# Performance work log

Hardware: AMD Instinct MI355X
Metric: run time of the kernel (lower is better)

The kernel has to match this reference:

```python
import jax, jax.numpy as jnp
import numpy as np

HIDDEN = 1024
HEADS = 16
DEPTH = HIDDEN // HEADS  # 64
B, F, T = 2, 2048, 2048


def setup_inputs() -> dict:
    key = jax.random.key(0)
    ks = jax.random.split(key, 7)
    return {
        "query_input": jax.random.normal(ks[0], (B, F, HIDDEN), dtype=jnp.float32),
        "source_input": jax.random.normal(ks[1], (B, T, HIDDEN), dtype=jnp.float32),
        "bias": jax.random.normal(ks[2], (1, 1, F, T), dtype=jnp.float32),
        "wq": jax.random.normal(ks[3], (HIDDEN, HEADS, DEPTH), dtype=jnp.float32) * 0.02,
        "wk": jax.random.normal(ks[4], (HIDDEN, HEADS, DEPTH), dtype=jnp.float32) * 0.02,
        "wv": jax.random.normal(ks[5], (HIDDEN, HEADS, DEPTH), dtype=jnp.float32) * 0.02,
        "wo": jax.random.normal(ks[6], (HEADS, DEPTH, HIDDEN), dtype=jnp.float32) * 0.02,
    }


def reference(query_input, source_input, bias, wq, wk, wv, wo):
    # projections: [B,S,C] x [C,N,H] -> [B,S,N,H]
    q = jnp.einsum("bfc,cnh->bfnh", query_input, wq)
    k = jnp.einsum("btc,cnh->btnh", source_input, wk)
    v = jnp.einsum("btc,cnh->btnh", source_input, wv)
    q = q * (DEPTH ** -0.5)
    # logits: [B,N,F,T], softmax over T (last dim)
    logits = jnp.einsum("btnh,bfnh->bnft", k, q)
    logits = logits + bias
    weights = jax.nn.softmax(logits, axis=3)
    attn = jnp.einsum("bnft,btnh->bfnh", weights, v)
    out = jnp.einsum("bfnh,nhe->bfe", attn, wo)
    return out
```

## Files before the change

kernel.cpp:

```cpp
#include <hip/hip_runtime.h>

#define LOG2E 1.44269504f

typedef __attribute__((ext_vector_type(8))) short short8v;
typedef __attribute__((ext_vector_type(4))) float f32x4;
typedef unsigned int u32;
typedef __attribute__((address_space(1))) const u32* gp_t;
typedef __attribute__((address_space(3))) u32* lp_t;

#define MFMA(a, b, c) __builtin_amdgcn_mfma_f32_16x16x32_bf16((a), (b), (c), 0, 0, 0)

__device__ __forceinline__ unsigned short f2bf(float f) {
  unsigned int u = __float_as_uint(f);
  u = (u + 0x7fffu + ((u >> 16) & 1u)) >> 16;
  return (unsigned short)u;
}
__device__ __forceinline__ u32 cvtpk(float lo, float hi) {
  u32 r;
  asm("v_cvt_pk_bf16_f32 %0, %1, %2" : "=v"(r) : "v"(lo), "v"(hi));
  return r;
}

__global__ void k_cvt2(const float* __restrict__ a, const float* __restrict__ bsrc,
                       unsigned short* __restrict__ oa, unsigned short* __restrict__ ob,
                       int n4each) {
  int stride = gridDim.x * blockDim.x;
  for (int i = blockIdx.x * blockDim.x + threadIdx.x; i < 2 * n4each; i += stride) {
    bool second = i >= n4each;
    int j = second ? i - n4each : i;
    float4 v = second ? reinterpret_cast<const float4*>(bsrc)[j]
                      : reinterpret_cast<const float4*>(a)[j];
    ushort4 o;
    o.x = f2bf(v.x); o.y = f2bf(v.y); o.z = f2bf(v.z); o.w = f2bf(v.w);
    (second ? reinterpret_cast<ushort4*>(ob) : reinterpret_cast<ushort4*>(oa))[j] = o;
  }
}

__global__ void k_cvt_t4(const float* __restrict__ w0, const float* __restrict__ w1,
                         const float* __restrict__ w2, const float* __restrict__ w3,
                         unsigned short* __restrict__ wqkvT, unsigned short* __restrict__ woT) {
  __shared__ float tile[32][33];
  int z = blockIdx.z;
  const float* in = (z == 0) ? w0 : (z == 1) ? w1 : (z == 2) ? w2 : w3;
  unsigned short* out = (z < 3) ? (wqkvT + (size_t)z * 1048576) : woT;
  float scale = (z == 0) ? 0.125f * LOG2E : 1.0f;
  int bx = blockIdx.x * 32, by = blockIdx.y * 32;
  int tx = threadIdx.x, ty = threadIdx.y;
  for (int r = ty; r < 32; r += 8)
    tile[r][tx] = in[(size_t)(by + r) * 1024 + bx + tx];
  __syncthreads();
  for (int r = ty; r < 32; r += 8)
    out[(size_t)(bx + r) * 1024 + by + tx] = f2bf(tile[tx][r] * scale);
}

__global__ void k_bias_perm(const float* __restrict__ in, float* __restrict__ out) {
  int bid = blockIdx.x;
  int fb = bid >> 5, ch = bid & 31;
  int tid = threadIdx.x;
  int tt = tid >> 6, rem = tid & 63;
  int g = rem >> 4, l15 = rem & 15;
  float4 v = *reinterpret_cast<const float4*>(
      &in[(size_t)(fb * 16 + l15) * 2048 + ch * 64 + tt * 16 + g * 4]);
  v.x *= LOG2E; v.y *= LOG2E; v.z *= LOG2E; v.w *= LOG2E;
  *reinterpret_cast<float4*>(&out[(size_t)bid * 1024 + tid * 4]) = v;
}

__global__ __launch_bounds__(256)
void k_gemmqkv(const unsigned short* __restrict__ Aq, const unsigned short* __restrict__ Asrc,
               const unsigned short* __restrict__ W,
               unsigned short* __restrict__ dq, unsigned short* __restrict__ dk,
               unsigned short* __restrict__ dv) {
  __shared__ __align__(16) unsigned short Al[2][8192];
  __shared__ __align__(16) unsigned short Bl[2][4096];
  const int tid = threadIdx.x;
  const int lane = tid & 63, wid = tid >> 6;
  const int g = lane >> 4, l15 = lane & 15, l7 = l15 & 7;
  const int wm = wid >> 1, wn = wid & 1;
  const int rowbase = blockIdx.y * 128;
  const int colbase = blockIdx.x * 64;
  const bool isV = colbase >= 2048;
  const unsigned short* A = (colbase < 1024) ? Aq : Asrc;
  const int xgl = (g ^ l7) << 4;

  const int jr = tid >> 3;
  const int sc = ((tid & 7) ^ (jr & 7)) << 3;
  const unsigned short* As0 = A + (size_t)(rowbase + jr) * 1024 + sc;
  const unsigned short* Ws0 = W + (size_t)(colbase + jr) * 1024 + sc;

  const f32x4 zf = {0.f, 0.f, 0.f, 0.f};
  f32x4 acc[4][2];
#pragma unroll
  for (int mf = 0; mf < 4; ++mf) { acc[mf][0] = zf; acc[mf][1] = zf; }

  auto stage = [&](int buf, int k0) {
    char* Ad = (char*)&Al[buf][0];
    char* Bd = (char*)&Bl[buf][0];
#pragma unroll
    for (int p = 0; p < 4; ++p)
      __builtin_amdgcn_global_load_lds((gp_t)(As0 + (size_t)p * 32 * 1024 + k0),
                                       (lp_t)(Ad + (p * 256 + tid) * 16), 16, 0, 0);
#pragma unroll
    for (int p = 0; p < 2; ++p)
      __builtin_amdgcn_global_load_lds((gp_t)(Ws0 + (size_t)p * 32 * 1024 + k0),
                                       (lp_t)(Bd + (p * 256 + tid) * 16), 16, 0, 0);
  };
  auto ldfrags = [&](int buf, int kk, short8v af[4], short8v bfr[2]) {
    const char* Ac = (const char*)&Al[buf][0];
    const char* Bc = (const char*)&Bl[buf][0];
#pragma unroll
    for (int mf = 0; mf < 4; ++mf)
      af[mf] = *reinterpret_cast<const short8v*>(
          Ac + ((wm * 64 + mf * 16 + l15) << 7) + (xgl ^ (kk << 6)));
#pragma unroll
    for (int nf = 0; nf < 2; ++nf)
      bfr[nf] = *reinterpret_cast<const short8v*>(
          Bc + ((wn * 32 + nf * 16 + l15) << 7) + (xgl ^ (kk << 6)));
  };

  stage(0, 0);
  __syncthreads();
#pragma unroll 1
  for (int s = 0; s < 16; ++s) {
    if (s < 15) stage((s + 1) & 1, (s + 1) * 64);
    __builtin_amdgcn_s_setprio(1);
    if (!isV) {
#pragma unroll
      for (int kk = 0; kk < 2; ++kk) {
        short8v af[4], bfr[2];
        ldfrags(s & 1, kk, af, bfr);
#pragma unroll
        for (int mf = 0; mf < 4; ++mf)
#pragma unroll
          for (int nf = 0; nf < 2; ++nf) acc[mf][nf] = MFMA(bfr[nf], af[mf], acc[mf][nf]);
      }
    } else {
#pragma unroll
      for (int kk = 0; kk < 2; ++kk) {
        short8v af[4], bfr[2];
        ldfrags(s & 1, kk, af, bfr);
#pragma unroll
        for (int mf = 0; mf < 4; ++mf)
#pragma unroll
          for (int nf = 0; nf < 2; ++nf) acc[mf][nf] = MFMA(af[mf], bfr[nf], acc[mf][nf]);
      }
    }
    __builtin_amdgcn_s_setprio(0);
    __syncthreads();
  }

  if (!isV) {
    unsigned short* dst = (colbase < 1024) ? dq : dk;
    const int cb = colbase & 1023;
#pragma unroll
    for (int mf = 0; mf < 4; ++mf)
#pragma unroll
      for (int nf = 0; nf < 2; ++nf) {
        f32x4 v = acc[mf][nf];
        int s = rowbase + wm * 64 + mf * 16 + l15;
        int c = cb + wn * 32 + nf * 16 + g * 4;
        int b = s >> 11, s2 = s & 2047, hd = c >> 6, h = c & 63;
        uint2 w; w.x = cvtpk(v[0], v[1]); w.y = cvtpk(v[2], v[3]);
        *reinterpret_cast<uint2*>(dst + ((size_t)(b * 16 + hd) * 2048 + s2) * 64 + h) = w;
      }
  } else {
    const int cb = colbase - 2048;
#pragma unroll
    for (int mf = 0; mf < 4; ++mf)
#pragma unroll
      for (int nf = 0; nf < 2; ++nf) {
        f32x4 v = acc[mf][nf];
        int s = rowbase + wm * 64 + mf * 16 + g * 4;
        int c = cb + wn * 32 + nf * 16 + l15;
        int b = s >> 11, s2 = s & 2047, hd = c >> 6, h = c & 63;
        uint2 w; w.x = cvtpk(v[0], v[1]); w.y = cvtpk(v[2], v[3]);
        *reinterpret_cast<uint2*>(dv + ((size_t)(b * 16 + hd) * 64 + h) * 2048 + s2) = w;
      }
  }
}

__global__ __launch_bounds__(256)
void k_gemmo(const unsigned short* __restrict__ A, const unsigned short* __restrict__ W,
             float* __restrict__ df) {
  __shared__ __align__(16) unsigned short Al[2][8192];
  __shared__ __align__(16) unsigned short Bl[2][4096];
  const int tid = threadIdx.x;
  const int lane = tid & 63, wid = tid >> 6;
  const int g = lane >> 4, l15 = lane & 15, l7 = l15 & 7;
  const int wm = wid >> 1, wn = wid & 1;
  const int rowbase = blockIdx.y * 128;
  const int colbase = blockIdx.x * 64;
  const int xgl = (g ^ l7) << 4;

  const int jr = tid >> 3;
  const int sc = ((tid & 7) ^ (jr & 7)) << 3;
  const unsigned short* As0 = A + (size_t)(rowbase + jr) * 1024 + sc;
  const unsigned short* Ws0 = W + (size_t)(colbase + jr) * 1024 + sc;

  const f32x4 zf = {0.f, 0.f, 0.f, 0.f};
  f32x4 acc[4][2];
#pragma unroll
  for (int mf = 0; mf < 4; ++mf) { acc[mf][0] = zf; acc[mf][1] = zf; }

  auto stage = [&](int buf, int k0) {
    char* Ad = (char*)&Al[buf][0];
    char* Bd = (char*)&Bl[buf][0];
#pragma unroll
    for (int p = 0; p < 4; ++p)
      __builtin_amdgcn_global_load_lds((gp_t)(As0 + (size_t)p * 32 * 1024 + k0),
                                       (lp_t)(Ad + (p * 256 + tid) * 16), 16, 0, 0);
#pragma unroll
    for (int p = 0; p < 2; ++p)
      __builtin_amdgcn_global_load_lds((gp_t)(Ws0 + (size_t)p * 32 * 1024 + k0),
                                       (lp_t)(Bd + (p * 256 + tid) * 16), 16, 0, 0);
  };

  stage(0, 0);
  __syncthreads();
#pragma unroll 1
  for (int s = 0; s < 16; ++s) {
    if (s < 15) stage((s + 1) & 1, (s + 1) * 64);
    const char* Ac = (const char*)&Al[s & 1][0];
    const char* Bc = (const char*)&Bl[s & 1][0];
    __builtin_amdgcn_s_setprio(1);
#pragma unroll
    for (int kk = 0; kk < 2; ++kk) {
      short8v af[4], bfr[2];
#pragma unroll
      for (int mf = 0; mf < 4; ++mf)
        af[mf] = *reinterpret_cast<const short8v*>(
            Ac + ((wm * 64 + mf * 16 + l15) << 7) + (xgl ^ (kk << 6)));
#pragma unroll
      for (int nf = 0; nf < 2; ++nf)
        bfr[nf] = *reinterpret_cast<const short8v*>(
            Bc + ((wn * 32 + nf * 16 + l15) << 7) + (xgl ^ (kk << 6)));
#pragma unroll
      for (int mf = 0; mf < 4; ++mf)
#pragma unroll
        for (int nf = 0; nf < 2; ++nf) acc[mf][nf] = MFMA(bfr[nf], af[mf], acc[mf][nf]);
    }
    __builtin_amdgcn_s_setprio(0);
    __syncthreads();
  }

#pragma unroll
  for (int mf = 0; mf < 4; ++mf)
#pragma unroll
    for (int nf = 0; nf < 2; ++nf) {
      int s = rowbase + wm * 64 + mf * 16 + l15;
      int c = colbase + wn * 32 + nf * 16 + g * 4;
      *reinterpret_cast<f32x4*>(df + (size_t)s * 1024 + c) = acc[mf][nf];
    }
}

__global__ __launch_bounds__(256, 2)
void k_attn(const unsigned short* __restrict__ qw,
            const unsigned short* __restrict__ kw,
            const unsigned short* __restrict__ vtw,
            const float* __restrict__ biaspf,
            unsigned short* __restrict__ attnb) {
  __shared__ __align__(16) unsigned short Kl[2][4096];
  __shared__ __align__(16) unsigned short Vl[2][4096];
  __shared__ __align__(16) unsigned short Pl[4][2048];

  const int tid = threadIdx.x;
  const int lane = tid & 63, wid = tid >> 6;
  const int g = lane >> 4, l15 = lane & 15, l7 = l15 & 7;
  const int xgl = (g ^ l7) << 4;

  const int bid = blockIdx.x;
  const int ft = bid >> 5, bn = bid & 31;
  const int b = bn >> 4, n = bn & 15;

  const size_t hoff = (size_t)bn * (2048 * 64);
  const unsigned short* qp = qw + hoff;
  const unsigned short* kp = kw + hoff;
  const unsigned short* vp = vtw + hoff;

  const int f0 = ft * 128 + wid * 32;
  const int fbb = ft * 8 + wid * 2;

  const int jr = tid >> 3;
  const int sc = ((tid & 7) ^ (jr & 7)) << 3;
  const unsigned short* Ks0 = kp + jr * 64 + sc;
  const unsigned short* Ks1 = kp + (jr + 32) * 64 + sc;
  const unsigned short* Vs0 = vp + jr * 2048 + sc;
  const unsigned short* Vs1 = vp + (jr + 32) * 2048 + sc;
  char* K0d = (char*)&Kl[0][0]; char* K1d = (char*)&Kl[1][0];
  char* V0d = (char*)&Vl[0][0]; char* V1d = (char*)&Vl[1][0];

  auto stage = [&](char* Kd, char* Vd, int ci) {
    int ko = ci << 12, vo = ci << 6;
    __builtin_amdgcn_global_load_lds((gp_t)(Ks0 + ko), (lp_t)(Kd + tid * 16), 16, 0, 0);
    __builtin_amdgcn_global_load_lds((gp_t)(Ks1 + ko), (lp_t)(Kd + 4096 + tid * 16), 16, 0, 0);
    __builtin_amdgcn_global_load_lds((gp_t)(Vs0 + vo), (lp_t)(Vd + tid * 16), 16, 0, 0);
    __builtin_amdgcn_global_load_lds((gp_t)(Vs1 + vo), (lp_t)(Vd + 4096 + tid * 16), 16, 0, 0);
  };

  short8v aq[2][2];
#pragma unroll
  for (int rg = 0; rg < 2; ++rg) {
    aq[rg][0] = *reinterpret_cast<const short8v*>(
        &qp[(size_t)(f0 + rg * 16 + l15) * 64 + g * 8]);
    aq[rg][1] = *reinterpret_cast<const short8v*>(
        &qp[(size_t)(f0 + rg * 16 + l15) * 64 + 32 + g * 8]);
  }

  const float* bias_lane = biaspf + (size_t)fbb * 32768 + lane * 4;

  const f32x4 zf = {0.f, 0.f, 0.f, 0.f};
  f32x4 o[2][4];
#pragma unroll
  for (int rg = 0; rg < 2; ++rg)
#pragma unroll
    for (int ht = 0; ht < 4; ++ht) o[rg][ht] = zf;
  float ls0 = 0.f, ls1 = 0.f;
  char* Pb = (char*)&Pl[wid][0] + l15 * 128;

  auto bload = [&](int ci, f32x4 bc[2][4]) {
#pragma unroll
    for (int rg = 0; rg < 2; ++rg)
#pragma unroll
      for (int tt = 0; tt < 4; ++tt)
        bc[rg][tt] = *reinterpret_cast<const f32x4*>(
            bias_lane + (size_t)rg * 32768 + ci * 1024 + tt * 256);
  };

  auto compute = [&](const unsigned short* Kb, const unsigned short* Vb,
                     const f32x4 bc[2][4]) {
    const char* Kc = (const char*)Kb; const char* Vc = (const char*)Vb;
    f32x4 st[2][4];
    __builtin_amdgcn_s_setprio(1);
#pragma unroll
    for (int tt = 0; tt < 4; ++tt) {
      short8v kb0 = *reinterpret_cast<const short8v*>(Kc + ((tt * 16 + l15) << 7) + xgl);
      short8v kb1 = *reinterpret_cast<const short8v*>(Kc + ((tt * 16 + l15) << 7) + (xgl ^ 64));
      st[0][tt] = MFMA(kb1, aq[0][1], MFMA(kb0, aq[0][0], bc[0][tt]));
      st[1][tt] = MFMA(kb1, aq[1][1], MFMA(kb0, aq[1][0], bc[1][tt]));
    }
    __builtin_amdgcn_s_setprio(0);

#pragma unroll
    for (int rg = 0; rg < 2; ++rg) {
      float rs = 0.f;
#pragma unroll
      for (int tt = 0; tt < 4; ++tt) {
        float p0 = __builtin_amdgcn_exp2f(st[rg][tt][0]);
        float p1 = __builtin_amdgcn_exp2f(st[rg][tt][1]);
        float p2 = __builtin_amdgcn_exp2f(st[rg][tt][2]);
        float p3 = __builtin_amdgcn_exp2f(st[rg][tt][3]);
        rs += (p0 + p1) + (p2 + p3);
        uint2 w;
        w.x = cvtpk(p0, p1);
        w.y = cvtpk(p2, p3);
        *reinterpret_cast<uint2*>(Pb + rg * 2048 + ((tt * 32 + g * 8) ^ (l7 * 16))) = w;
      }
      rs += __shfl_xor(rs, 16);
      rs += __shfl_xor(rs, 32);
      if (rg == 0) ls0 += rs; else ls1 += rs;
    }

    __builtin_amdgcn_s_setprio(1);
#pragma unroll
    for (int c = 0; c < 2; ++c) {
      short8v pa0 = *reinterpret_cast<const short8v*>(Pb + ((c << 6) ^ xgl));
      short8v pa1 = *reinterpret_cast<const short8v*>(Pb + 2048 + ((c << 6) ^ xgl));
#pragma unroll
      for (int ht = 0; ht < 4; ++ht) {
        short8v vb = *reinterpret_cast<const short8v*>(
            Vc + ((ht * 16 + l15) << 7) + (xgl ^ (c << 6)));
        o[0][ht] = MFMA(pa0, vb, o[0][ht]);
        o[1][ht] = MFMA(pa1, vb, o[1][ht]);
      }
    }
    __builtin_amdgcn_s_setprio(0);
  };

  f32x4 cb[2][4], nb[2][4];
  stage(K0d, V0d, 0);
  bload(0, cb);
  __syncthreads();
#pragma unroll 1
  for (int ci = 0; ci < 32; ci += 2) {
    stage(K1d, V1d, (ci + 1) & 31);
    bload((ci + 1) & 31, nb);
    compute(Kl[0], Vl[0], cb);
#pragma unroll
    for (int rg = 0; rg < 2; ++rg)
#pragma unroll
      for (int q = 0; q < 4; ++q) cb[rg][q] = nb[rg][q];
    __syncthreads();
    stage(K0d, V0d, (ci + 2) & 31);
    bload((ci + 2) & 31, nb);
    compute(Kl[1], Vl[1], cb);
#pragma unroll
    for (int rg = 0; rg < 2; ++rg)
#pragma unroll
      for (int q = 0; q < 4; ++q) cb[rg][q] = nb[rg][q];
    __syncthreads();
  }

#pragma unroll
  for (int rg = 0; rg < 2; ++rg) {
    float inv = 1.f / (rg == 0 ? ls0 : ls1);
    float i0 = __shfl(inv, g * 4 + 0, 16);
    float i1 = __shfl(inv, g * 4 + 1, 16);
    float i2 = __shfl(inv, g * 4 + 2, 16);
    float i3 = __shfl(inv, g * 4 + 3, 16);
#pragma unroll
    for (int ht = 0; ht < 4; ++ht) {
      unsigned short* ob = &attnb[((size_t)b * 2048 + f0 + rg * 16 + g * 4) * 1024 +
                                  n * 64 + ht * 16 + l15];
      ob[0] = f2bf(o[rg][ht][0] * i0);
      ob[1024] = f2bf(o[rg][ht][1] * i1);
      ob[2048] = f2bf(o[rg][ht][2] * i2);
      ob[3072] = f2bf(o[rg][ht][3] * i3);
    }
  }
}

extern "C" void kernel_launch(void* const* d_in, const int* in_sizes, int n_in,
                              void* d_out, int out_size, void* d_ws, size_t ws_size,
                              hipStream_t stream) {
  const float* query  = (const float*)d_in[0];
  const float* source = (const float*)d_in[1];
  const float* bias   = (const float*)d_in[2];
  const float* wq     = (const float*)d_in[3];
  const float* wk     = (const float*)d_in[4];
  const float* wv     = (const float*)d_in[5];
  const float* wo     = (const float*)d_in[6];

  char* ws = (char*)d_ws;
  unsigned short* qin_b  = (unsigned short*)(ws + 0);
  unsigned short* src_b  = (unsigned short*)(ws + 8388608);
  float*          bias_f = (float*)(ws + 0);
  unsigned short* wqkvT  = (unsigned short*)(ws + 16777216);
  unsigned short* woT    = (unsigned short*)(ws + 23068672);
  unsigned short* q_ws   = (unsigned short*)(ws + 25165824);
  unsigned short* k_ws   = (unsigned short*)(ws + 33554432);
  unsigned short* vT_ws  = (unsigned short*)(ws + 41943040);
  unsigned short* attn_b = (unsigned short*)(ws + 50331648);

  k_cvt2<<<2048, 256, 0, stream>>>(query, source, qin_b, src_b, 1048576);
  dim3 tb(32, 8);
  k_cvt_t4<<<dim3(32, 32, 4), tb, 0, stream>>>(wq, wk, wv, wo, wqkvT, woT);

  k_gemmqkv<<<dim3(48, 32), 256, 0, stream>>>(qin_b, src_b, wqkvT, q_ws, k_ws, vT_ws);
  k_bias_perm<<<4096, 256, 0, stream>>>(bias, bias_f);
  k_attn<<<512, 256, 0, stream>>>(q_ws, k_ws, vT_ws, bias_f, attn_b);
  k_gemmo<<<dim3(16, 32), 256, 0, stream>>>(attn_b, woT, (float*)d_out);
}
```

Baseline: 138.6 us.

## Triple-buffer K/V LDS staging with partial vmcnt waits in attention loop

Expands the K/V shared-memory staging from double to triple buffering so loads run two chunks ahead of compute. The full __syncthreads is replaced by an explicit s_waitcnt vmcnt(4) plus s_barrier, which waits only for the older chunk's loads while the newer ones stay in flight. Scheduling barriers pin the ordering of the bias loads, staging and compute. The extra buffer adds LDS use, which could limit the two-blocks-per-CU occupancy, and correctness depends on the hand-counted vmcnt matching the outstanding loads.

```diff
diff --git a/kernel.cpp b/kernel.cpp
--- a/kernel.cpp
+++ b/kernel.cpp
@@ -258,8 +258,8 @@
             const unsigned short* __restrict__ vtw,
             const float* __restrict__ biaspf,
             unsigned short* __restrict__ attnb) {
-  __shared__ __align__(16) unsigned short Kl[2][4096];
-  __shared__ __align__(16) unsigned short Vl[2][4096];
+  __shared__ __align__(16) unsigned short Kl[3][4096];
+  __shared__ __align__(16) unsigned short Vl[3][4096];
   __shared__ __align__(16) unsigned short Pl[4][2048];
 
   const int tid = threadIdx.x;
@@ -285,10 +285,10 @@
   const unsigned short* Ks1 = kp + (jr + 32) * 64 + sc;
   const unsigned short* Vs0 = vp + jr * 2048 + sc;
   const unsigned short* Vs1 = vp + (jr + 32) * 2048 + sc;
-  char* K0d = (char*)&Kl[0][0]; char* K1d = (char*)&Kl[1][0];
-  char* V0d = (char*)&Vl[0][0]; char* V1d = (char*)&Vl[1][0];
-
-  auto stage = [&](char* Kd, char* Vd, int ci) {
+
+  auto stage = [&](int buf, int ci) {
+    char* Kd = (char*)&Kl[buf][0];
+    char* Vd = (char*)&Vl[buf][0];
     int ko = ci << 12, vo = ci << 6;
     __builtin_amdgcn_global_load_lds((gp_t)(Ks0 + ko), (lp_t)(Kd + tid * 16), 16, 0, 0);
     __builtin_amdgcn_global_load_lds((gp_t)(Ks1 + ko), (lp_t)(Kd + 4096 + tid * 16), 16, 0, 0);
@@ -325,9 +325,9 @@
             bias_lane + (size_t)rg * 32768 + ci * 1024 + tt * 256);
   };
 
-  auto compute = [&](const unsigned short* Kb, const unsigned short* Vb,
-                     const f32x4 bc[2][4]) {
-    const char* Kc = (const char*)Kb; const char* Vc = (const char*)Vb;
+  auto compute = [&](int buf, const f32x4 bc[2][4]) {
+    const char* Kc = (const char*)&Kl[buf][0];
+    const char* Vc = (const char*)&Vl[buf][0];
     f32x4 st[2][4];
     __builtin_amdgcn_s_setprio(1);
 #pragma unroll
@@ -376,27 +376,32 @@
   };
 
   f32x4 cb[2][4], nb[2][4];
-  stage(K0d, V0d, 0);
   bload(0, cb);
-  __syncthreads();
+  __builtin_amdgcn_sched_barrier(0);
+  stage(0, 0);
+  stage(1, 1);
+  asm volatile("s_waitcnt vmcnt(4)" ::: "memory");
+  __builtin_amdgcn_sched_barrier(0);
+  __builtin_amdgcn_s_barrier();
+  __builtin_amdgcn_sched_barrier(0);
+
+  int cur = 0;
 #pragma unroll 1
-  for (int ci = 0; ci < 32; ci += 2) {
-    stage(K1d, V1d, (ci + 1) & 31);
+  for (int ci = 0; ci < 32; ++ci) {
     bload((ci + 1) & 31, nb);
-    compute(Kl[0], Vl[0], cb);
+    __builtin_amdgcn_sched_barrier(0);
+    int nxt = cur + 2; if (nxt >= 3) nxt -= 3;
+    stage(nxt, (ci + 2) & 31);
+    compute(cur, cb);
+    asm volatile("s_waitcnt vmcnt(4)" ::: "memory");
+    __builtin_amdgcn_sched_barrier(0);
+    __builtin_amdgcn_s_barrier();
+    __builtin_amdgcn_sched_barrier(0);
 #pragma unroll
     for (int rg = 0; rg < 2; ++rg)
 #pragma unroll
       for (int q = 0; q < 4; ++q) cb[rg][q] = nb[rg][q];
-    __syncthreads();
-    stage(K0d, V0d, (ci + 2) & 31);
-    bload((ci + 2) & 31, nb);
-    compute(Kl[1], Vl[1], cb);
-#pragma unroll
-    for (int rg = 0; rg < 2; ++rg)
-#pragma unroll
-      for (int q = 0; q < 4; ++q) cb[rg][q] = nb[rg][q];
-    __syncthreads();
+    ++cur; if (cur >= 3) cur -= 3;
   }
 
 #pragma unroll
```

After: 142.1 us. 1.03x slower.

## Process two KV chunks per barrier phase with interleaved QK and PV

Applied to the files above, without the earlier changes.

The attention loop now stages two 64-key chunks per phase into a doubled LDS double-buffer, so there is one barrier per two chunks instead of one per chunk. Within a phase, both chunks' QK MFMAs are issued back to back with the bias prefetches placed between them. The softmax and PV steps follow, which gives the scheduler more independent work to overlap exp and LDS traffic with matrix ops. The cost is doubled K/V LDS footprint (about 48KB total) and more live registers for a second score and bias set, which may threaten the 2-blocks-per-CU occupancy target.

```diff
diff --git a/kernel.cpp b/kernel.cpp
--- a/kernel.cpp
+++ b/kernel.cpp
@@ -258,8 +258,8 @@
             const unsigned short* __restrict__ vtw,
             const float* __restrict__ biaspf,
             unsigned short* __restrict__ attnb) {
-  __shared__ __align__(16) unsigned short Kl[2][4096];
-  __shared__ __align__(16) unsigned short Vl[2][4096];
+  __shared__ __align__(16) unsigned short Kl[2][2][4096];
+  __shared__ __align__(16) unsigned short Vl[2][2][4096];
   __shared__ __align__(16) unsigned short Pl[4][2048];
 
   const int tid = threadIdx.x;
@@ -285,15 +285,19 @@
   const unsigned short* Ks1 = kp + (jr + 32) * 64 + sc;
   const unsigned short* Vs0 = vp + jr * 2048 + sc;
   const unsigned short* Vs1 = vp + (jr + 32) * 2048 + sc;
-  char* K0d = (char*)&Kl[0][0]; char* K1d = (char*)&Kl[1][0];
-  char* V0d = (char*)&Vl[0][0]; char* V1d = (char*)&Vl[1][0];
-
-  auto stage = [&](char* Kd, char* Vd, int ci) {
-    int ko = ci << 12, vo = ci << 6;
-    __builtin_amdgcn_global_load_lds((gp_t)(Ks0 + ko), (lp_t)(Kd + tid * 16), 16, 0, 0);
-    __builtin_amdgcn_global_load_lds((gp_t)(Ks1 + ko), (lp_t)(Kd + 4096 + tid * 16), 16, 0, 0);
-    __builtin_amdgcn_global_load_lds((gp_t)(Vs0 + vo), (lp_t)(Vd + tid * 16), 16, 0, 0);
-    __builtin_amdgcn_global_load_lds((gp_t)(Vs1 + vo), (lp_t)(Vd + 4096 + tid * 16), 16, 0, 0);
+
+  auto stage_pair = [&](int pb, int pi) {
+#pragma unroll
+    for (int s = 0; s < 2; ++s) {
+      int ci = 2 * pi + s;
+      char* Kd = (char*)&Kl[pb][s][0];
+      char* Vd = (char*)&Vl[pb][s][0];
+      int ko = ci << 12, vo = ci << 6;
+      __builtin_amdgcn_global_load_lds((gp_t)(Ks0 + ko), (lp_t)(Kd + tid * 16), 16, 0, 0);
+      __builtin_amdgcn_global_load_lds((gp_t)(Ks1 + ko), (lp_t)(Kd + 4096 + tid * 16), 16, 0, 0);
+      __builtin_amdgcn_global_load_lds((gp_t)(Vs0 + vo), (lp_t)(Vd + tid * 16), 16, 0, 0);
+      __builtin_amdgcn_global_load_lds((gp_t)(Vs1 + vo), (lp_t)(Vd + 4096 + tid * 16), 16, 0, 0);
+    }
   };
 
   short8v aq[2][2];
@@ -325,10 +329,7 @@
             bias_lane + (size_t)rg * 32768 + ci * 1024 + tt * 256);
   };
 
-  auto compute = [&](const unsigned short* Kb, const unsigned short* Vb,
-                     const f32x4 bc[2][4]) {
-    const char* Kc = (const char*)Kb; const char* Vc = (const char*)Vb;
-    f32x4 st[2][4];
+  auto qk = [&](const char* Kc, const f32x4 bc[2][4], f32x4 st[2][4]) {
     __builtin_amdgcn_s_setprio(1);
 #pragma unroll
     for (int tt = 0; tt < 4; ++tt) {
@@ -338,7 +339,9 @@
       st[1][tt] = MFMA(kb1, aq[1][1], MFMA(kb0, aq[1][0], bc[1][tt]));
     }
     __builtin_amdgcn_s_setprio(0);
-
+  };
+
+  auto sm = [&](const f32x4 st[2][4]) {
 #pragma unroll
     for (int rg = 0; rg < 2; ++rg) {
       float rs = 0.f;
@@ -358,7 +361,9 @@
       rs += __shfl_xor(rs, 32);
       if (rg == 0) ls0 += rs; else ls1 += rs;
     }
-
+  };
+
+  auto pv = [&](const char* Vc) {
     __builtin_amdgcn_s_setprio(1);
 #pragma unroll
     for (int c = 0; c < 2; ++c) {
@@ -375,28 +380,36 @@
     __builtin_amdgcn_s_setprio(0);
   };
 
-  f32x4 cb[2][4], nb[2][4];
-  stage(K0d, V0d, 0);
-  bload(0, cb);
+  f32x4 cbA[2][4], cbB[2][4], nbA[2][4], nbB[2][4];
+  stage_pair(0, 0);
+  bload(0, cbA);
+  bload(1, cbB);
   __syncthreads();
+
 #pragma unroll 1
-  for (int ci = 0; ci < 32; ci += 2) {
-    stage(K1d, V1d, (ci + 1) & 31);
-    bload((ci + 1) & 31, nb);
-    compute(Kl[0], Vl[0], cb);
+  for (int ph = 0; ph < 16; ++ph) {
+    const int pb = ph & 1;
+    if (ph < 15) stage_pair(pb ^ 1, ph + 1);
+    const char* K0 = (const char*)&Kl[pb][0][0];
+    const char* K1 = (const char*)&Kl[pb][1][0];
+    const char* V0 = (const char*)&Vl[pb][0][0];
+    const char* V1 = (const char*)&Vl[pb][1][0];
+
+    f32x4 stA[2][4], stB[2][4];
+    qk(K0, cbA, stA);
+    if (ph < 15) bload(2 * ph + 2, nbA);
+    qk(K1, cbB, stB);
+    if (ph < 15) bload(2 * ph + 3, nbB);
+    sm(stA);
+    pv(V0);
+    sm(stB);
+    pv(V1);
+
+    __syncthreads();
 #pragma unroll
     for (int rg = 0; rg < 2; ++rg)
 #pragma unroll
-      for (int q = 0; q < 4; ++q) cb[rg][q] = nb[rg][q];
-    __syncthreads();
-    stage(K0d, V0d, (ci + 2) & 31);
-    bload((ci + 2) & 31, nb);
-    compute(Kl[1], Vl[1], cb);
-#pragma unroll
-    for (int rg = 0; rg < 2; ++rg)
-#pragma unroll
-      for (int q = 0; q < 4; ++q) cb[rg][q] = nb[rg][q];
-    __syncthreads();
+      for (int q = 0; q < 4; ++q) { cbA[rg][q] = nbA[rg][q]; cbB[rg][q] = nbB[rg][q]; }
   }
 
 #pragma unroll
```

New measurement: 138.8 us. Within noise of the previous version (+0.1%).
